# Kernel optimization log

Measured on AMD Instinct MI355X. Metric: run time of the kernel, lower is better.

Reference implementation:

```python
import jax, jax.numpy as jnp
import numpy as np
from jax import lax

INPUT_SIZE = 16
HIDDEN = 32
CHANNELS = 12
LP_NORM = 2.0
POOL_K = 3
POOL_S = 2
# nn.RReLU in eval mode uses the fixed slope (lower+upper)/2 for negative inputs
RRELU_SLOPE = (0.125 + 0.333) / 2.0


def setup_inputs() -> dict:
    key = jax.random.key(0)
    ks = jax.random.split(key, 8)
    x = jax.random.normal(ks[0], (4096, 2048, INPUT_SIZE), dtype=jnp.float32)
    bound_rnn = 1.0 / np.sqrt(HIDDEN)
    W_ih = jax.random.uniform(ks[1], (HIDDEN, INPUT_SIZE), jnp.float32, -bound_rnn, bound_rnn)
    W_hh = jax.random.uniform(ks[2], (HIDDEN, HIDDEN), jnp.float32, -bound_rnn, bound_rnn)
    b_ih = jax.random.uniform(ks[3], (HIDDEN,), jnp.float32, -bound_rnn, bound_rnn)
    b_hh = jax.random.uniform(ks[4], (HIDDEN,), jnp.float32, -bound_rnn, bound_rnn)
    bound_p = 1.0 / np.sqrt(HIDDEN)
    W_proj = jax.random.uniform(ks[5], (CHANNELS, HIDDEN), jnp.float32, -bound_p, bound_p)
    b_proj = jax.random.uniform(ks[6], (CHANNELS,), jnp.float32, -bound_p, bound_p)
    return {"x": x, "W_ih": W_ih, "W_hh": W_hh, "b_ih": b_ih, "b_hh": b_hh,
            "W_proj": W_proj, "b_proj": b_proj}


def reference(x, W_ih, W_hh, b_ih, b_hh, W_proj, b_proj):
    B, T, F = x.shape
    h0 = jnp.zeros((B, HIDDEN), dtype=x.dtype)

    def step(h, xt):
        # RNNCell (tanh); note the *pre-RReLU* hidden state is carried forward
        h_new = jnp.tanh(xt @ W_ih.T + b_ih + h @ W_hh.T + b_hh)
        h_act = jnp.where(h_new >= 0, h_new, h_new * RRELU_SLOPE)  # eval-mode RReLU
        p = h_act @ W_proj.T + b_proj  # (B, C)
        return h_new, p

    _, ps = lax.scan(step, h0, jnp.transpose(x, (1, 0, 2)))  # ps: (T, B, C)
    stacked = jnp.transpose(ps, (1, 2, 0))  # (B, C, T)

    # LPPool1d with p=2: (sum over window of x^p)^(1/p)
    powed = stacked * stacked
    summed = lax.reduce_window(powed, 0.0, lax.add,
                               window_dimensions=(1, 1, POOL_K),
                               window_strides=(1, 1, POOL_S),
                               padding=((0, 0), (0, 0), (0, 0)))
    pooled = jnp.sqrt(summed)  # (B, C, L_out)
    return jnp.max(pooled, axis=1)  # (B, L_out)
```

## Files before the change

kernel.cpp:

```cpp
#include <hip/hip_runtime.h>
#include <math.h>

#define T_LEN   2048
#define B_ROWS  4096
#define F_IN    16
#define HID     32
#define NCH     12
#define L_OUT   1023
#define TCH     8
#define NCHUNK  (T_LEN / TCH)
#define RRELU_SLOPE 0.229f
#define ZSCALE  2.8853900817779268f

typedef _Float16 half4 __attribute__((ext_vector_type(4)));
typedef _Float16 half8 __attribute__((ext_vector_type(8)));
typedef float    f32x4 __attribute__((ext_vector_type(4)));

__device__ __forceinline__ f32x4 mfma16(half4 a, half4 b, f32x4 c) {
    return __builtin_amdgcn_mfma_f32_16x16x16f16(a, b, c, 0, 0, 0);
}

__device__ __forceinline__ f32x4 hmfma32(half8 a, half8 b, f32x4 c) {
#if __has_builtin(__builtin_amdgcn_mfma_f32_16x16x32_f16)
    return __builtin_amdgcn_mfma_f32_16x16x32_f16(a, b, c, 0, 0, 0);
#else
    const uint4 ua = __builtin_bit_cast(uint4, a);
    const uint4 ub = __builtin_bit_cast(uint4, b);
    uint2 t;
    t.x = ua.x; t.y = ua.y; const half4 alo = __builtin_bit_cast(half4, t);
    t.x = ua.z; t.y = ua.w; const half4 ahi = __builtin_bit_cast(half4, t);
    t.x = ub.x; t.y = ub.y; const half4 blo = __builtin_bit_cast(half4, t);
    t.x = ub.z; t.y = ub.w; const half4 bhi = __builtin_bit_cast(half4, t);
    return mfma16(ahi, bhi, mfma16(alo, blo, c));
#endif
}

__device__ __forceinline__ float act_fast(float zs) {
    float e = __builtin_amdgcn_exp2f(zs);
    float r = __builtin_amdgcn_rcpf(e + 1.0f);
    return fmaf(-2.0f, r, 1.0f);
}

__device__ __forceinline__ unsigned pk2u(float a, float b) {
    return __builtin_bit_cast(unsigned, __builtin_amdgcn_cvt_pkrtz(a, b));
}
__device__ __forceinline__ half4 pack4(float a, float b, float c, float d) {
    uint2 u; u.x = pk2u(a, b); u.y = pk2u(c, d);
    return __builtin_bit_cast(half4, u);
}

__device__ __forceinline__ uint4 u4(f32x4 v) { return __builtin_bit_cast(uint4, v); }
__device__ __forceinline__ f32x4 f4(uint4 v) { return __builtin_bit_cast(f32x4, v); }

__global__ __launch_bounds__(192, 1)
void rnn_mfma_kernel(const float* __restrict__ x,
                     const float* __restrict__ W_ih,
                     const float* __restrict__ W_hh,
                     const float* __restrict__ b_ih,
                     const float* __restrict__ b_hh,
                     const float* __restrict__ W_proj,
                     const float* __restrict__ b_proj,
                     float* __restrict__ out)
{
    __shared__ alignas(16) uint4 hqs[2][TCH][64];
    __shared__ alignas(16) uint4 xza_s[2][TCH][64];
    __shared__ alignas(16) uint4 xzb_s[2][TCH][64];
    __shared__ alignas(16) float pbuf[64];

    const int tid  = threadIdx.x;
    const int wid  = tid >> 6;
    const int lane = tid & 63;
    const int c16  = lane & 15;
    const int g    = lane >> 4;
    const int rowBase = blockIdx.x * 16;

    const f32x4 zero4 = {0.0f, 0.0f, 0.0f, 0.0f};

    const float4* xsrc = (const float4*)x;
    const size_t xrow = (size_t)(rowBase + c16) * T_LEN;
    float* outrow = out + (size_t)(rowBase + c16) * L_OUT;

    half8 AhhF[2];
    half4 Aih[2];
    half8 ApF;
    f32x4 biasA = zero4, biasB = zero4, biasP = zero4;
    float4 xsA[TCH], xsB[TCH];

    if (wid == 0) {
        #pragma unroll
        for (int U = 0; U < 2; ++U) {
            half8 f;
            #pragma unroll
            for (int V = 0; V < 2; ++V)
                #pragma unroll
                for (int i = 0; i < 4; ++i)
                    f[V*4 + i] = (_Float16)(ZSCALE *
                        W_hh[(U*16 + c16)*HID + V*16 + 4*g + i]);
            AhhF[U] = f;
        }
    } else if (wid == 1) {
        #pragma unroll
        for (int U = 0; U < 2; ++U)
            #pragma unroll
            for (int i = 0; i < 4; ++i)
                Aih[U][i] = (_Float16)(ZSCALE *
                    W_ih[(U*16 + c16)*F_IN + 4*g + i]);
        #pragma unroll
        for (int r = 0; r < 4; ++r) {
            const int u = 4*g + r;
            biasA[r] = ZSCALE * (b_ih[u]      + b_hh[u]);
            biasB[r] = ZSCALE * (b_ih[16 + u] + b_hh[16 + u]);
        }
    } else {
        #pragma unroll
        for (int V = 0; V < 2; ++V)
            #pragma unroll
            for (int i = 0; i < 4; ++i)
                ApF[V*4 + i] = (c16 < NCH)
                    ? (_Float16)W_proj[c16*HID + V*16 + 4*g + i]
                    : (_Float16)0.0f;
        #pragma unroll
        for (int r = 0; r < 4; ++r) {
            const int u = 4*g + r;
            biasP[r] = (u < NCH) ? b_proj[u] : 0.0f;
        }
    }

    half8 Bh = {0,0,0,0,0,0,0,0};
    f32x4 Wc = zero4;

    auto w1_load = [&](int c, float4* xs) {
        const int cc = (c < NCHUNK) ? c : NCHUNK - 1;
        #pragma unroll
        for (int m = 0; m < TCH; ++m)
            xs[m] = xsrc[(xrow + cc*TCH + m) * 4 + g];
    };
    auto w1_compute = [&](int buf, const float4* xs) {
        #pragma unroll
        for (int m = 0; m < TCH; ++m) {
            const half4 Bx = pack4(xs[m].x, xs[m].y, xs[m].z, xs[m].w);
            xza_s[buf][m][lane] = u4(mfma16(Aih[0], Bx, biasA));
            xzb_s[buf][m][lane] = u4(mfma16(Aih[1], Bx, biasB));
        }
    };

    auto w0_chunk = [&](int buf) {
        uint4 ra[TCH], rb[TCH];
        #pragma unroll
        for (int i = 0; i < TCH; ++i) {
            ra[i] = xza_s[buf][i][lane];
            rb[i] = xzb_s[buf][i][lane];
        }
        #pragma unroll
        for (int tt = 0; tt < TCH; ++tt) {
            const f32x4 za = hmfma32(AhhF[0], Bh, f4(ra[tt]));
            const f32x4 zb = hmfma32(AhhF[1], Bh, f4(rb[tt]));
            uint4 hp;
            hp.x = pk2u(act_fast(za[0]), act_fast(za[1]));
            hp.y = pk2u(act_fast(za[2]), act_fast(za[3]));
            hp.z = pk2u(act_fast(zb[0]), act_fast(zb[1]));
            hp.w = pk2u(act_fast(zb[2]), act_fast(zb[3]));
            Bh = __builtin_bit_cast(half8, hp);
            hqs[buf][tt][lane] = hp;
        }
    };

    const half8 sl8 = {(_Float16)RRELU_SLOPE, (_Float16)RRELU_SLOPE,
                       (_Float16)RRELU_SLOPE, (_Float16)RRELU_SLOPE,
                       (_Float16)RRELU_SLOPE, (_Float16)RRELU_SLOPE,
                       (_Float16)RRELU_SLOPE, (_Float16)RRELU_SLOPE};
    auto w2_process = [&](int c, int buf) {
        #pragma unroll
        for (int tt = 0; tt < TCH; ++tt) {
            const int t = c*TCH + tt;
            const uint4 hv = hqs[buf][tt][lane];
            const half8 h8 = __builtin_bit_cast(half8, hv);
            const half8 a8 = __builtin_elementwise_max(h8, h8 * sl8);
            const f32x4 p  = hmfma32(ApF, a8, biasP);
            const f32x4 q4 = p * p;
            if ((tt & 1) == 0) {
                const f32x4 pr = Wc + q4;
                if (t >= 2) {
                    const float mloc = fmaxf(fmaxf(pr[0], pr[1]),
                                             fmaxf(pr[2], pr[3]));
                    pbuf[c16*4 + g] = mloc;
                    if (g == 0) {
                        const f32x4 pv = *(const f32x4*)&pbuf[c16*4];
                        const float mm = fmaxf(fmaxf(pv[0], pv[1]),
                                               fmaxf(pv[2], pv[3]));
                        outrow[(t >> 1) - 1] = __builtin_amdgcn_sqrtf(mm);
                    }
                }
                Wc = q4;
            } else {
                Wc = Wc + q4;
            }
        }
    };

    if (wid == 1) {
        w1_load(0, xsA);
        w1_compute(0, xsA);
        w1_load(1, xsA);
    }
    __syncthreads();

    for (int cc = 0; cc < NCHUNK; cc += 2) {
        if (wid == 0) {
            w0_chunk(0);
        } else if (wid == 1) {
            w1_load(cc + 2, xsB);
            w1_compute(1, xsA);
        } else {
            if (cc > 0) w2_process(cc - 1, 1);
        }
        __syncthreads();
        if (wid == 0) {
            w0_chunk(1);
        } else if (wid == 1) {
            w1_load(cc + 3, xsA);
            w1_compute(0, xsB);
        } else {
            w2_process(cc, 0);
        }
        __syncthreads();
    }
    if (wid == 2) w2_process(NCHUNK - 1, 1);
}

extern "C" void kernel_launch(void* const* d_in, const int* in_sizes, int n_in,
                              void* d_out, int out_size, void* d_ws, size_t ws_size,
                              hipStream_t stream) {
    const float* x      = (const float*)d_in[0];
    const float* W_ih   = (const float*)d_in[1];
    const float* W_hh   = (const float*)d_in[2];
    const float* b_ih   = (const float*)d_in[3];
    const float* b_hh   = (const float*)d_in[4];
    const float* W_proj = (const float*)d_in[5];
    const float* b_proj = (const float*)d_in[6];
    float* out = (float*)d_out;

    dim3 grid(B_ROWS / 16);
    dim3 block(192);
    hipLaunchKernelGGL(rnn_mfma_kernel, grid, block, 0, stream,
                       x, W_ih, W_hh, b_ih, b_hh, W_proj, b_proj, out);
}
```

Before: 319.2 us.

## Split recurrent step across two waves with per-timestep barrier exchange

The serial recurrence is split so two wavefronts each compute half of the hidden units (one 16x16x32 MFMA each) and swap halves through shared memory at every timestep, using a lightweight lgkmcnt-wait plus s_barrier. The x-projection and output waves are interleaved at timestep granularity instead of per chunk, and the tanh uses a shared reciprocal for pairs of values. This is meant to shorten the latency of each recurrent step, at the cost of a block-wide barrier on every timestep and an extra LDS round trip on the critical path.

```diff
diff --git a/kernel.cpp b/kernel.cpp
--- a/kernel.cpp
+++ b/kernel.cpp
@@ -35,12 +35,6 @@
 #endif
 }
 
-__device__ __forceinline__ float act_fast(float zs) {
-    float e = __builtin_amdgcn_exp2f(zs);
-    float r = __builtin_amdgcn_rcpf(e + 1.0f);
-    return fmaf(-2.0f, r, 1.0f);
-}
-
 __device__ __forceinline__ unsigned pk2u(float a, float b) {
     return __builtin_bit_cast(unsigned, __builtin_amdgcn_cvt_pkrtz(a, b));
 }
@@ -48,11 +42,12 @@
     uint2 u; u.x = pk2u(a, b); u.y = pk2u(c, d);
     return __builtin_bit_cast(half4, u);
 }
-
 __device__ __forceinline__ uint4 u4(f32x4 v) { return __builtin_bit_cast(uint4, v); }
 __device__ __forceinline__ f32x4 f4(uint4 v) { return __builtin_bit_cast(f32x4, v); }
 
-__global__ __launch_bounds__(192, 1)
+#define STEP_SYNC() asm volatile("s_waitcnt lgkmcnt(0)\n\ts_barrier" ::: "memory")
+
+__global__ __launch_bounds__(256, 1)
 void rnn_mfma_kernel(const float* __restrict__ x,
                      const float* __restrict__ W_ih,
                      const float* __restrict__ W_hh,
@@ -75,36 +70,31 @@
     const int rowBase = blockIdx.x * 16;
 
     const f32x4 zero4 = {0.0f, 0.0f, 0.0f, 0.0f};
-
     const float4* xsrc = (const float4*)x;
     const size_t xrow = (size_t)(rowBase + c16) * T_LEN;
     float* outrow = out + (size_t)(rowBase + c16) * L_OUT;
 
-    half8 AhhF[2];
+    const int U = wid;
+    half8 AhhF = {0,0,0,0,0,0,0,0};
     half4 Aih[2];
     half8 ApF;
     f32x4 biasA = zero4, biasB = zero4, biasP = zero4;
     float4 xsA[TCH], xsB[TCH];
 
-    if (wid == 0) {
-        #pragma unroll
-        for (int U = 0; U < 2; ++U) {
-            half8 f;
-            #pragma unroll
-            for (int V = 0; V < 2; ++V)
-                #pragma unroll
-                for (int i = 0; i < 4; ++i)
-                    f[V*4 + i] = (_Float16)(ZSCALE *
-                        W_hh[(U*16 + c16)*HID + V*16 + 4*g + i]);
-            AhhF[U] = f;
-        }
-    } else if (wid == 1) {
-        #pragma unroll
-        for (int U = 0; U < 2; ++U)
+    if (wid <= 1) {
+        #pragma unroll
+        for (int V = 0; V < 2; ++V)
             #pragma unroll
             for (int i = 0; i < 4; ++i)
-                Aih[U][i] = (_Float16)(ZSCALE *
-                    W_ih[(U*16 + c16)*F_IN + 4*g + i]);
+                AhhF[V*4 + i] = (_Float16)(ZSCALE *
+                    W_hh[(U*16 + c16)*HID + V*16 + 4*g + i]);
+    } else if (wid == 2) {
+        #pragma unroll
+        for (int Uu = 0; Uu < 2; ++Uu)
+            #pragma unroll
+            for (int i = 0; i < 4; ++i)
+                Aih[Uu][i] = (_Float16)(ZSCALE *
+                    W_ih[(Uu*16 + c16)*F_IN + 4*g + i]);
         #pragma unroll
         for (int r = 0; r < 4; ++r) {
             const int u = 4*g + r;
@@ -127,105 +117,118 @@
     }
 
     half8 Bh = {0,0,0,0,0,0,0,0};
+    uint4 xz_cur;
     f32x4 Wc = zero4;
-
-    auto w1_load = [&](int c, float4* xs) {
-        const int cc = (c < NCHUNK) ? c : NCHUNK - 1;
-        #pragma unroll
-        for (int m = 0; m < TCH; ++m)
-            xs[m] = xsrc[(xrow + cc*TCH + m) * 4 + g];
-    };
-    auto w1_compute = [&](int buf, const float4* xs) {
-        #pragma unroll
-        for (int m = 0; m < TCH; ++m) {
-            const half4 Bx = pack4(xs[m].x, xs[m].y, xs[m].z, xs[m].w);
-            xza_s[buf][m][lane] = u4(mfma16(Aih[0], Bx, biasA));
-            xzb_s[buf][m][lane] = u4(mfma16(Aih[1], Bx, biasB));
-        }
-    };
-
-    auto w0_chunk = [&](int buf) {
-        uint4 ra[TCH], rb[TCH];
-        #pragma unroll
-        for (int i = 0; i < TCH; ++i) {
-            ra[i] = xza_s[buf][i][lane];
-            rb[i] = xzb_s[buf][i][lane];
-        }
-        #pragma unroll
-        for (int tt = 0; tt < TCH; ++tt) {
-            const f32x4 za = hmfma32(AhhF[0], Bh, f4(ra[tt]));
-            const f32x4 zb = hmfma32(AhhF[1], Bh, f4(rb[tt]));
-            uint4 hp;
-            hp.x = pk2u(act_fast(za[0]), act_fast(za[1]));
-            hp.y = pk2u(act_fast(za[2]), act_fast(za[3]));
-            hp.z = pk2u(act_fast(zb[0]), act_fast(zb[1]));
-            hp.w = pk2u(act_fast(zb[2]), act_fast(zb[3]));
-            Bh = __builtin_bit_cast(half8, hp);
-            hqs[buf][tt][lane] = hp;
-        }
+    const uint4* xz_base = (U == 0) ? &xza_s[0][0][0] : &xzb_s[0][0][0];
+
+    auto w0_compute = [&](int buf, int tt) {
+        const f32x4 z = hmfma32(AhhF, Bh, f4(xz_cur));
+        const int nbuf = (tt < TCH-1) ? buf : (buf ^ 1);
+        const int ntt  = (tt < TCH-1) ? tt + 1 : 0;
+        xz_cur = xz_base[(nbuf*TCH + ntt)*64 + lane];
+        const float e0 = __builtin_amdgcn_exp2f(z[0]);
+        const float e1 = __builtin_amdgcn_exp2f(z[1]);
+        const float e2 = __builtin_amdgcn_exp2f(z[2]);
+        const float e3 = __builtin_amdgcn_exp2f(z[3]);
+        const float d0 = e0 + 1.0f, d1 = e1 + 1.0f;
+        const float d2 = e2 + 1.0f, d3 = e3 + 1.0f;
+        const float r01 = __builtin_amdgcn_rcpf(d0 * d1);
+        const float r23 = __builtin_amdgcn_rcpf(d2 * d3);
+        const float i0 = d1 * r01, i1 = d0 * r01;
+        const float i2 = d3 * r23, i3 = d2 * r23;
+        const float h0 = fmaf(-2.0f, i0, 1.0f);
+        const float h1 = fmaf(-2.0f, i1, 1.0f);
+        const float h2 = fmaf(-2.0f, i2, 1.0f);
+        const float h3 = fmaf(-2.0f, i3, 1.0f);
+        uint2 own; own.x = pk2u(h0, h1); own.y = pk2u(h2, h3);
+        ((uint2*)&hqs[buf][tt][lane])[U] = own;
+    };
+    auto w0_after = [&](int buf, int tt) {
+        Bh = __builtin_bit_cast(half8, hqs[buf][tt][lane]);
+    };
+
+    auto w1_slot = [&](int buf, int tt, const float4* xs_use, float4* xs_fill,
+                       int loadchunk) {
+        const int cc2 = (loadchunk < NCHUNK) ? loadchunk : NCHUNK - 1;
+        xs_fill[tt] = xsrc[(xrow + (size_t)cc2*TCH + tt) * 4 + g];
+        const half4 Bx = pack4(xs_use[tt].x, xs_use[tt].y,
+                               xs_use[tt].z, xs_use[tt].w);
+        xza_s[buf][tt][lane] = u4(mfma16(Aih[0], Bx, biasA));
+        xzb_s[buf][tt][lane] = u4(mfma16(Aih[1], Bx, biasB));
     };
 
     const half8 sl8 = {(_Float16)RRELU_SLOPE, (_Float16)RRELU_SLOPE,
                        (_Float16)RRELU_SLOPE, (_Float16)RRELU_SLOPE,
                        (_Float16)RRELU_SLOPE, (_Float16)RRELU_SLOPE,
                        (_Float16)RRELU_SLOPE, (_Float16)RRELU_SLOPE};
-    auto w2_process = [&](int c, int buf) {
+    auto w2_slot = [&](int c, int buf, int tt) {
+        const int t = c*TCH + tt;
+        const uint4 hv = hqs[buf][tt][lane];
+        const half8 h8 = __builtin_bit_cast(half8, hv);
+        const half8 a8 = __builtin_elementwise_max(h8, h8 * sl8);
+        const f32x4 p  = hmfma32(ApF, a8, biasP);
+        const f32x4 q4 = p * p;
+        if ((tt & 1) == 0) {
+            const f32x4 pr = Wc + q4;
+            if (t >= 2) {
+                const float mloc = fmaxf(fmaxf(pr[0], pr[1]),
+                                         fmaxf(pr[2], pr[3]));
+                pbuf[c16*4 + g] = mloc;
+                if (g == 0) {
+                    const f32x4 pv = *(const f32x4*)&pbuf[c16*4];
+                    const float mm = fmaxf(fmaxf(pv[0], pv[1]),
+                                           fmaxf(pv[2], pv[3]));
+                    outrow[(t >> 1) - 1] = __builtin_amdgcn_sqrtf(mm);
+                }
+            }
+            Wc = q4;
+        } else {
+            Wc = Wc + q4;
+        }
+    };
+
+    if (wid == 2) {
+        float4 x0[TCH];
+        #pragma unroll
+        for (int m = 0; m < TCH; ++m)
+            x0[m] = xsrc[(xrow + m) * 4 + g];
+        #pragma unroll
+        for (int m = 0; m < TCH; ++m) {
+            const half4 Bx = pack4(x0[m].x, x0[m].y, x0[m].z, x0[m].w);
+            xza_s[0][m][lane] = u4(mfma16(Aih[0], Bx, biasA));
+            xzb_s[0][m][lane] = u4(mfma16(Aih[1], Bx, biasB));
+        }
+        #pragma unroll
+        for (int m = 0; m < TCH; ++m)
+            xsA[m] = xsrc[(xrow + TCH + m) * 4 + g];
+    }
+    STEP_SYNC();
+    if (wid <= 1)
+        xz_cur = xz_base[lane];
+
+    for (int cc = 0; cc < NCHUNK; cc += 2) {
         #pragma unroll
         for (int tt = 0; tt < TCH; ++tt) {
-            const int t = c*TCH + tt;
-            const uint4 hv = hqs[buf][tt][lane];
-            const half8 h8 = __builtin_bit_cast(half8, hv);
-            const half8 a8 = __builtin_elementwise_max(h8, h8 * sl8);
-            const f32x4 p  = hmfma32(ApF, a8, biasP);
-            const f32x4 q4 = p * p;
-            if ((tt & 1) == 0) {
-                const f32x4 pr = Wc + q4;
-                if (t >= 2) {
-                    const float mloc = fmaxf(fmaxf(pr[0], pr[1]),
-                                             fmaxf(pr[2], pr[3]));
-                    pbuf[c16*4 + g] = mloc;
-                    if (g == 0) {
-                        const f32x4 pv = *(const f32x4*)&pbuf[c16*4];
-                        const float mm = fmaxf(fmaxf(pv[0], pv[1]),
-                                               fmaxf(pv[2], pv[3]));
-                        outrow[(t >> 1) - 1] = __builtin_amdgcn_sqrtf(mm);
-                    }
-                }
-                Wc = q4;
-            } else {
-                Wc = Wc + q4;
-            }
-        }
-    };
-
-    if (wid == 1) {
-        w1_load(0, xsA);
-        w1_compute(0, xsA);
-        w1_load(1, xsA);
-    }
-    __syncthreads();
-
-    for (int cc = 0; cc < NCHUNK; cc += 2) {
-        if (wid == 0) {
-            w0_chunk(0);
-        } else if (wid == 1) {
-            w1_load(cc + 2, xsB);
-            w1_compute(1, xsA);
-        } else {
-            if (cc > 0) w2_process(cc - 1, 1);
-        }
-        __syncthreads();
-        if (wid == 0) {
-            w0_chunk(1);
-        } else if (wid == 1) {
-            w1_load(cc + 3, xsA);
-            w1_compute(0, xsB);
-        } else {
-            w2_process(cc, 0);
-        }
-        __syncthreads();
-    }
-    if (wid == 2) w2_process(NCHUNK - 1, 1);
+            if (wid <= 1)        w0_compute(0, tt);
+            else if (wid == 2)   w1_slot(1, tt, xsA, xsB, cc + 2);
+            else if (cc > 0)     w2_slot(cc - 1, 1, tt);
+            STEP_SYNC();
+            if (wid <= 1)        w0_after(0, tt);
+        }
+        #pragma unroll
+        for (int tt = 0; tt < TCH; ++tt) {
+            if (wid <= 1)        w0_compute(1, tt);
+            else if (wid == 2)   w1_slot(0, tt, xsB, xsA, cc + 3);
+            else                 w2_slot(cc, 0, tt);
+            STEP_SYNC();
+            if (wid <= 1)        w0_after(1, tt);
+        }
+    }
+    if (wid == 3) {
+        #pragma unroll
+        for (int tt = 0; tt < TCH; ++tt)
+            w2_slot(NCHUNK - 1, 1, tt);
+    }
 }
 
 extern "C" void kernel_launch(void* const* d_in, const int* in_sizes, int n_in,
@@ -241,7 +244,7 @@
     float* out = (float*)d_out;
 
     dim3 grid(B_ROWS / 16);
-    dim3 block(192);
+    dim3 block(256);
     hipLaunchKernelGGL(rnn_mfma_kernel, grid, block, 0, stream,
                        x, W_ih, W_hh, b_ih, b_hh, W_proj, b_proj, out);
 }
```

Result: slower. 686.7 us (+115.2%).
